# Kernel tuning notes

Hardware: AMD Instinct MI355X
Metric: run time of the kernel (lower is better)

Reference implementation:

```python
import math
import jax, jax.numpy as jnp
import numpy as np

B, T, C = 2, 2048, 2048
H, G = 16, 4          # n_head, n_group
HKV = H // G          # kv heads
HD = C // H           # head dim = 128

def setup_inputs() -> dict:
    key = jax.random.key(0)
    ks = jax.random.split(key, 4)
    s = 0.02  # realistic init scale
    return {
        "x": jax.random.normal(ks[0], (B, T, C), jnp.float32),
        "Wkv": jax.random.normal(ks[1], (C, 2 * C // G), jnp.float32) * s,
        "bkv": jnp.zeros((2 * C // G,), jnp.float32),
        "Wq": jax.random.normal(ks[2], (C, C), jnp.float32) * s,
        "bq": jnp.zeros((C,), jnp.float32),
        "Wp": jax.random.normal(ks[3], (C, C), jnp.float32) * s,
        "bp": jnp.zeros((C,), jnp.float32),
    }

def _expand_kv(t):
    # (B,T,HKV*HD) -> replicate each kv head G times -> (B,H,T,HD)
    t = t.reshape(B, T, HKV, HD)
    t = jnp.broadcast_to(t[:, :, None], (B, T, G, HKV, HD)).reshape(B, T, H, HD)
    return t.transpose(0, 2, 1, 3)

def reference(x, Wkv, bkv, Wq, bq, Wp, bp):
    kv = x @ Wkv + bkv                      # (B,T,2C/G)
    k, v = jnp.split(kv, 2, axis=-1)
    q = (x @ Wq + bq).reshape(B, T, H, HD).transpose(0, 2, 1, 3)  # (B,H,T,HD)
    k = _expand_kv(k)
    v = _expand_kv(v)
    att = jnp.einsum('bhqd,bhkd->bhqk', q, k) * (1.0 / math.sqrt(HD))
    mask = jnp.tril(jnp.ones((T, T), bool))
    att = jnp.where(mask, att, -jnp.inf)
    att = jax.nn.softmax(att, axis=-1)
    y = jnp.einsum('bhqk,bhkd->bhqd', att, v)
    y = y.transpose(0, 2, 1, 3).reshape(B, T, C)
    return y @ Wp + bp
```

## Files before the change

### kernel.cpp

```cpp
#include <hip/hip_runtime.h>

#define Bv 2
#define Tv 2048
#define Cv 2048
#define Hv 16
#define HKVv 4
#define HDv 128

typedef __attribute__((ext_vector_type(8))) __bf16 bf16x8;
typedef __attribute__((ext_vector_type(4))) float floatx4;

__device__ __forceinline__ unsigned short f2b(float f) {
  unsigned int x = __float_as_uint(f);
  x += 0x7fffu + ((x >> 16) & 1u);
  return (unsigned short)(x >> 16);
}

#define MFMA(a, b, c) __builtin_amdgcn_mfma_f32_16x16x32_bf16((a), (b), (c), 0, 0, 0)

__device__ __forceinline__ void gld_lds16(const void* g, void* l) {
  __builtin_amdgcn_global_load_lds((const __attribute__((address_space(1))) void*)g,
                                   (__attribute__((address_space(3))) void*)l, 16, 0, 0);
}

__global__ void cvt_kernel(const float* __restrict__ src, unsigned short* __restrict__ dst, int n4) {
  int i = blockIdx.x * blockDim.x + threadIdx.x;
  if (i < n4) {
    float4 f = ((const float4*)src)[i];
    ushort4 u;
    u.x = f2b(f.x); u.y = f2b(f.y); u.z = f2b(f.z); u.w = f2b(f.w);
    ((ushort4*)dst)[i] = u;
  }
}

__global__ void tcvt_kernel(const float* __restrict__ src, unsigned short* __restrict__ dst, int K, int N) {
  __shared__ float tile[32][33];
  int k0 = blockIdx.x * 32, n0 = blockIdx.y * 32;
  int tx = threadIdx.x, ty = threadIdx.y;
  for (int i = ty; i < 32; i += 8)
    tile[i][tx] = src[(size_t)(k0 + i) * N + n0 + tx];
  __syncthreads();
  for (int i = ty; i < 32; i += 8)
    dst[(size_t)(n0 + i) * K + k0 + tx] = f2b(tile[tx][i]);
}

__global__ __launch_bounds__(256) void gemm_qkv(
    const unsigned short* __restrict__ xb,
    const unsigned short* __restrict__ wq_t,
    const unsigned short* __restrict__ wkv_t,
    const float* __restrict__ bq, const float* __restrict__ bkv,
    unsigned short* __restrict__ qs,
    unsigned short* __restrict__ ks,
    unsigned short* __restrict__ vs) {
  __shared__ __align__(16) unsigned short Ash[2][128 * 32];
  __shared__ __align__(16) unsigned short Bsh[2][128 * 32];
  int tid = threadIdx.x;
  int wave = tid >> 6, lane = tid & 63;
  int c = lane & 15, quad = lane >> 4;
  int wr = (wave >> 1) * 64, wc = (wave & 1) * 64;
  int m0 = blockIdx.x * 128, n0 = blockIdx.y * 128;
  bool isq = (n0 < 2048);
  const unsigned short* wt = isq ? (wq_t + (size_t)n0 * 2048)
                                 : (wkv_t + (size_t)(n0 - 2048) * 2048);
  floatx4 zero4 = {0.f, 0.f, 0.f, 0.f};
  floatx4 acc[4][4];
#pragma unroll
  for (int i = 0; i < 4; i++)
#pragma unroll
    for (int j = 0; j < 4; j++) acc[i][j] = zero4;

  const unsigned short* Abase = xb + (size_t)m0 * 2048;
  int s0 = wave * 128 + lane, s1 = wave * 128 + 64 + lane;
  int r0 = s0 >> 2, kc0 = (s0 & 3) ^ (r0 & 3);
  int r1 = s1 >> 2, kc1 = (s1 & 3) ^ (r1 & 3);
  int swz3 = quad ^ (c & 3);
  int dA0 = (wave * 128) * 8, dA1 = (wave * 128 + 64) * 8;

  gld_lds16(Abase + (size_t)r0 * 2048 + kc0 * 8, &Ash[0][0] + dA0);
  gld_lds16(Abase + (size_t)r1 * 2048 + kc1 * 8, &Ash[0][0] + dA1);
  gld_lds16(wt + (size_t)r0 * 2048 + kc0 * 8, &Bsh[0][0] + dA0);
  gld_lds16(wt + (size_t)r1 * 2048 + kc1 * 8, &Bsh[0][0] + dA1);
  __syncthreads();

  for (int it = 0; it < 64; it++) {
    int cur = it & 1;
    if (it + 1 < 64) {
      int k1 = (it + 1) * 32;
      gld_lds16(Abase + (size_t)r0 * 2048 + k1 + kc0 * 8, &Ash[cur ^ 1][0] + dA0);
      gld_lds16(Abase + (size_t)r1 * 2048 + k1 + kc1 * 8, &Ash[cur ^ 1][0] + dA1);
      gld_lds16(wt + (size_t)r0 * 2048 + k1 + kc0 * 8, &Bsh[cur ^ 1][0] + dA0);
      gld_lds16(wt + (size_t)r1 * 2048 + k1 + kc1 * 8, &Bsh[cur ^ 1][0] + dA1);
    }
    bf16x8 af[4], bfv[4];
#pragma unroll
    for (int i = 0; i < 4; i++)
      af[i] = *(const bf16x8*)(&Ash[cur][(wr + i * 16 + c) * 32 + swz3 * 8]);
#pragma unroll
    for (int j = 0; j < 4; j++)
      bfv[j] = *(const bf16x8*)(&Bsh[cur][(wc + j * 16 + c) * 32 + swz3 * 8]);
#pragma unroll
    for (int i = 0; i < 4; i++)
#pragma unroll
      for (int j = 0; j < 4; j++)
        acc[i][j] = MFMA(af[i], bfv[j], acc[i][j]);
    __syncthreads();
  }

#pragma unroll
  for (int i = 0; i < 4; i++) {
#pragma unroll
    for (int j = 0; j < 4; j++) {
#pragma unroll
      for (int r = 0; r < 4; r++) {
        int m = m0 + wr + i * 16 + quad * 4 + r;
        int n = n0 + wc + j * 16 + c;
        int bidx = m >> 11, t = m & 2047;
        float val = acc[i][j][r];
        if (isq) {
          val = (val + bq[n]) * 0.08838834764831845f;
          int hh = n >> 7, d = n & 127;
          qs[((size_t)((bidx * Hv + hh) * Tv) + t) * HDv + d] = f2b(val);
        } else {
          int n2 = n - 2048;
          val += bkv[n2];
          if (n2 < 512) {
            int hh = n2 >> 7, d = n2 & 127;
            ks[((size_t)((bidx * HKVv + hh) * Tv) + t) * HDv + d] = f2b(val);
          } else {
            int n3 = n2 - 512;
            int hh = n3 >> 7, d = n3 & 127;
            vs[((size_t)((bidx * HKVv + hh) * HDv) + d) * Tv + t] = f2b(val);
          }
        }
      }
    }
  }
}

__global__ __launch_bounds__(256, 4) void attn_kernel(
    const unsigned short* __restrict__ qs,
    const unsigned short* __restrict__ ks,
    const unsigned short* __restrict__ vs,
    unsigned short* __restrict__ ys) {
  __shared__ __align__(16) unsigned short Ksh[2][32 * 128];
  __shared__ __align__(16) unsigned short Vsh[2][128 * 32];
  __shared__ __align__(16) unsigned short Psh[4][16 * 32];

  int x = blockIdx.x, h = blockIdx.y, b = blockIdx.z;
  int qt = (h & 8) ? (31 - x) : x;
  int hkv = h & (HKVv - 1);
  int tid = threadIdx.x;
  int wave = tid >> 6, lane = tid & 63;
  int c = lane & 15, quad = lane >> 4;
  int q0w = qt * 64 + wave * 16;
  int qrow = q0w + c;
  int swzK = c & 7, swzV = c & 3;

  const unsigned short* qptr = qs + ((size_t)((b * Hv + h) * Tv) + q0w) * HDv;
  const unsigned short* kbase = ks + (size_t)((b * HKVv + hkv) * Tv) * HDv;
  const unsigned short* vbase = vs + (size_t)((b * HKVv + hkv) * HDv) * Tv;

  bf16x8 qf[4];
#pragma unroll
  for (int kc = 0; kc < 4; kc++)
    qf[kc] = *(const bf16x8*)(qptr + (size_t)c * HDv + kc * 32 + quad * 8);

  floatx4 zero4 = {0.f, 0.f, 0.f, 0.f};
  floatx4 o[8];
#pragma unroll
  for (int dt = 0; dt < 8; dt++) o[dt] = zero4;
  float M = -1e30f, L = 0.f;

  unsigned short* Pw = &Psh[wave][0];

  int kOff[2], vOff[2];
#pragma unroll
  for (int i = 0; i < 2; i++) {
    int s = wave * 128 + i * 64 + lane;
    int rk = s >> 4, gk = (s & 15) ^ (rk & 7);
    kOff[i] = rk * 128 + gk * 8;
    int rv = s >> 2, gv = (s & 3) ^ (rv & 3);
    vOff[i] = rv * Tv + gv * 8;
  }
  int ldsBase = (wave * 128) * 8;

  int ntiles = 2 * qt + 2;

#pragma unroll
  for (int i = 0; i < 2; i++) gld_lds16(kbase + kOff[i], &Ksh[0][0] + ldsBase + i * 512);
#pragma unroll
  for (int i = 0; i < 2; i++) gld_lds16(vbase + vOff[i], &Vsh[0][0] + ldsBase + i * 512);
  __syncthreads();

  for (int kt = 0; kt < ntiles; kt++) {
    int kv0 = kt * 32;
    int cur = kt & 1;
    if (kt + 1 < ntiles) {
      int kv1 = (kt + 1) * 32;
#pragma unroll
      for (int i = 0; i < 2; i++)
        gld_lds16(kbase + (size_t)kv1 * 128 + kOff[i], &Ksh[cur ^ 1][0] + ldsBase + i * 512);
#pragma unroll
      for (int i = 0; i < 2; i++)
        gld_lds16(vbase + kv1 + vOff[i], &Vsh[cur ^ 1][0] + ldsBase + i * 512);
    }

    if (kv0 <= q0w + 15) {
      const unsigned short* Kb = &Ksh[cur][0];
      const unsigned short* Vb = &Vsh[cur][0];
      floatx4 st[2] = {zero4, zero4};
#pragma unroll
      for (int kc = 0; kc < 4; kc++) {
#pragma unroll
        for (int sub = 0; sub < 2; sub++) {
          bf16x8 kf = *(const bf16x8*)(&Kb[(sub * 16 + c) * 128 + (((kc * 4 + quad) ^ swzK) * 8)]);
          st[sub] = MFMA(kf, qf[kc], st[sub]);
        }
      }
      if (kv0 + 31 > q0w) {
#pragma unroll
        for (int sub = 0; sub < 2; sub++) {
          int kvb = kv0 + sub * 16 + quad * 4;
#pragma unroll
          for (int r = 0; r < 4; r++)
            if (kvb + r > qrow) st[sub][r] = -1e30f;
        }
      }
      float mx = -1e30f;
#pragma unroll
      for (int sub = 0; sub < 2; sub++)
        mx = fmaxf(mx, fmaxf(fmaxf(st[sub][0], st[sub][1]), fmaxf(st[sub][2], st[sub][3])));
      mx = fmaxf(mx, __shfl_xor(mx, 16));
      mx = fmaxf(mx, __shfl_xor(mx, 32));
      float Mn = fmaxf(M, mx);
      float al = __expf(M - Mn);
      M = Mn;
      float l = 0.f;
#pragma unroll
      for (int sub = 0; sub < 2; sub++) {
        float p0 = __expf(st[sub][0] - Mn);
        float p1 = __expf(st[sub][1] - Mn);
        float p2 = __expf(st[sub][2] - Mn);
        float p3 = __expf(st[sub][3] - Mn);
        l += (p0 + p1) + (p2 + p3);
        unsigned int lo = (unsigned int)f2b(p0) | ((unsigned int)f2b(p1) << 16);
        unsigned int hi = (unsigned int)f2b(p2) | ((unsigned int)f2b(p3) << 16);
        int g = (sub * 2 + (quad >> 1)) ^ swzV;
        *(uint2*)(&Pw[c * 32 + g * 8 + (quad & 1) * 4]) = make_uint2(lo, hi);
      }
      l += __shfl_xor(l, 16);
      l += __shfl_xor(l, 32);
      L = L * al + l;
#pragma unroll
      for (int dt = 0; dt < 8; dt++) o[dt] *= al;
      bf16x8 pf = *(const bf16x8*)(&Pw[c * 32 + ((quad ^ swzV) * 8)]);
#pragma unroll
      for (int dt = 0; dt < 8; dt++) {
        bf16x8 vf = *(const bf16x8*)(&Vb[(dt * 16 + c) * 32 + ((quad ^ swzV) * 8)]);
        o[dt] = MFMA(vf, pf, o[dt]);
      }
    }
    __syncthreads();
  }

  float Li = 1.0f / L;
  size_t rowbase = ((size_t)(b * Tv + qrow)) * Cv + h * HDv;
#pragma unroll
  for (int dt = 0; dt < 8; dt++) {
    unsigned int lo = (unsigned int)f2b(o[dt][0] * Li) | ((unsigned int)f2b(o[dt][1] * Li) << 16);
    unsigned int hi2 = (unsigned int)f2b(o[dt][2] * Li) | ((unsigned int)f2b(o[dt][3] * Li) << 16);
    *(uint2*)(&ys[rowbase + dt * 16 + quad * 4]) = make_uint2(lo, hi2);
  }
}

__global__ __launch_bounds__(256) void gemm_proj(
    const unsigned short* __restrict__ ys,
    const unsigned short* __restrict__ wp_t,
    const float* __restrict__ bp,
    float* __restrict__ out) {
  __shared__ __align__(16) unsigned short Ash[2][128 * 32];
  __shared__ __align__(16) unsigned short Bsh[2][128 * 32];
  int tid = threadIdx.x;
  int wave = tid >> 6, lane = tid & 63;
  int c = lane & 15, quad = lane >> 4;
  int wr = (wave >> 1) * 64, wc = (wave & 1) * 64;
  int m0 = blockIdx.x * 128, n0 = blockIdx.y * 128;
  floatx4 zero4 = {0.f, 0.f, 0.f, 0.f};
  floatx4 acc[4][4];
#pragma unroll
  for (int i = 0; i < 4; i++)
#pragma unroll
    for (int j = 0; j < 4; j++) acc[i][j] = zero4;

  const unsigned short* Abase = ys + (size_t)m0 * 2048;
  const unsigned short* Bbase = wp_t + (size_t)n0 * 2048;
  int s0 = wave * 128 + lane, s1 = wave * 128 + 64 + lane;
  int r0 = s0 >> 2, kc0 = (s0 & 3) ^ (r0 & 3);
  int r1 = s1 >> 2, kc1 = (s1 & 3) ^ (r1 & 3);
  int swz3 = quad ^ (c & 3);
  int dA0 = (wave * 128) * 8, dA1 = (wave * 128 + 64) * 8;

  gld_lds16(Abase + (size_t)r0 * 2048 + kc0 * 8, &Ash[0][0] + dA0);
  gld_lds16(Abase + (size_t)r1 * 2048 + kc1 * 8, &Ash[0][0] + dA1);
  gld_lds16(Bbase + (size_t)r0 * 2048 + kc0 * 8, &Bsh[0][0] + dA0);
  gld_lds16(Bbase + (size_t)r1 * 2048 + kc1 * 8, &Bsh[0][0] + dA1);
  __syncthreads();

  for (int it = 0; it < 64; it++) {
    int cur = it & 1;
    if (it + 1 < 64) {
      int k1 = (it + 1) * 32;
      gld_lds16(Abase + (size_t)r0 * 2048 + k1 + kc0 * 8, &Ash[cur ^ 1][0] + dA0);
      gld_lds16(Abase + (size_t)r1 * 2048 + k1 + kc1 * 8, &Ash[cur ^ 1][0] + dA1);
      gld_lds16(Bbase + (size_t)r0 * 2048 + k1 + kc0 * 8, &Bsh[cur ^ 1][0] + dA0);
      gld_lds16(Bbase + (size_t)r1 * 2048 + k1 + kc1 * 8, &Bsh[cur ^ 1][0] + dA1);
    }
    bf16x8 af[4], bfv[4];
#pragma unroll
    for (int i = 0; i < 4; i++)
      af[i] = *(const bf16x8*)(&Ash[cur][(wr + i * 16 + c) * 32 + swz3 * 8]);
#pragma unroll
    for (int j = 0; j < 4; j++)
      bfv[j] = *(const bf16x8*)(&Bsh[cur][(wc + j * 16 + c) * 32 + swz3 * 8]);
#pragma unroll
    for (int i = 0; i < 4; i++)
#pragma unroll
      for (int j = 0; j < 4; j++)
        acc[i][j] = MFMA(af[i], bfv[j], acc[i][j]);
    __syncthreads();
  }

#pragma unroll
  for (int i = 0; i < 4; i++) {
#pragma unroll
    for (int j = 0; j < 4; j++) {
#pragma unroll
      for (int r = 0; r < 4; r++) {
        int m = m0 + wr + i * 16 + quad * 4 + r;
        int n = n0 + wc + j * 16 + c;
        out[(size_t)m * 2048 + n] = acc[i][j][r] + bp[n];
      }
    }
  }
}

extern "C" void kernel_launch(void* const* d_in, const int* in_sizes, int n_in,
                              void* d_out, int out_size, void* d_ws, size_t ws_size,
                              hipStream_t stream) {
  (void)in_sizes; (void)n_in; (void)out_size; (void)ws_size;
  const float* x   = (const float*)d_in[0];
  const float* Wkv = (const float*)d_in[1];
  const float* bkv = (const float*)d_in[2];
  const float* Wq  = (const float*)d_in[3];
  const float* bq  = (const float*)d_in[4];
  const float* Wp  = (const float*)d_in[5];
  const float* bp  = (const float*)d_in[6];
  float* out = (float*)d_out;

  char* ws = (char*)d_ws;
  unsigned short* xb    = (unsigned short*)(ws + 0);
  unsigned short* wq_t  = (unsigned short*)(ws + 16777216);
  unsigned short* wkv_t = (unsigned short*)(ws + 25165824);
  unsigned short* wp_t  = (unsigned short*)(ws + 29360128);
  unsigned short* qs    = (unsigned short*)(ws + 37748736);
  unsigned short* ks    = (unsigned short*)(ws + 54525952);
  unsigned short* vs    = (unsigned short*)(ws + 58720256);
  unsigned short* ysbuf = (unsigned short*)(ws + 62914560);

  cvt_kernel<<<8192, 256, 0, stream>>>(x, xb, 2097152);
  tcvt_kernel<<<dim3(64, 64), dim3(32, 8), 0, stream>>>(Wq, wq_t, 2048, 2048);
  tcvt_kernel<<<dim3(64, 32), dim3(32, 8), 0, stream>>>(Wkv, wkv_t, 2048, 1024);
  tcvt_kernel<<<dim3(64, 64), dim3(32, 8), 0, stream>>>(Wp, wp_t, 2048, 2048);
  gemm_qkv<<<dim3(32, 24), 256, 0, stream>>>(xb, wq_t, wkv_t, bq, bkv, qs, ks, vs);
  attn_kernel<<<dim3(32, 16, 2), 256, 0, stream>>>(qs, ks, vs, ysbuf);
  gemm_proj<<<dim3(32, 16), 256, 0, stream>>>(ysbuf, wp_t, bp, out);
}
```

Measured before the change: 349.6 us.

## Switch attention to 32x32x16 MFMA with register-shuffled P, merge weight converts

```diff
diff --git a/kernel.cpp b/kernel.cpp
--- a/kernel.cpp
+++ b/kernel.cpp
@@ -8,7 +8,9 @@
 #define HDv 128
 
 typedef __attribute__((ext_vector_type(8))) __bf16 bf16x8;
+typedef __attribute__((ext_vector_type(4))) __bf16 bf16x4;
 typedef __attribute__((ext_vector_type(4))) float floatx4;
+typedef __attribute__((ext_vector_type(16))) float floatx16;
 
 __device__ __forceinline__ unsigned short f2b(float f) {
   unsigned int x = __float_as_uint(f);
@@ -17,6 +19,7 @@
 }
 
 #define MFMA(a, b, c) __builtin_amdgcn_mfma_f32_16x16x32_bf16((a), (b), (c), 0, 0, 0)
+#define MFMA32(a, b, c) __builtin_amdgcn_mfma_f32_32x32x16_bf16((a), (b), (c), 0, 0, 0)
 
 __device__ __forceinline__ void gld_lds16(const void* g, void* l) {
   __builtin_amdgcn_global_load_lds((const __attribute__((address_space(1))) void*)g,
@@ -33,15 +36,23 @@
   }
 }
 
-__global__ void tcvt_kernel(const float* __restrict__ src, unsigned short* __restrict__ dst, int K, int N) {
+__global__ void tcvt3_kernel(const float* __restrict__ Wq, const float* __restrict__ Wkv,
+                             const float* __restrict__ Wp,
+                             unsigned short* __restrict__ wq_t, unsigned short* __restrict__ wkv_t,
+                             unsigned short* __restrict__ wp_t) {
   __shared__ float tile[32][33];
+  int which = blockIdx.z;
+  const float* src = (which == 0) ? Wq : (which == 1) ? Wkv : Wp;
+  unsigned short* dst = (which == 0) ? wq_t : (which == 1) ? wkv_t : wp_t;
+  int N = (which == 1) ? 1024 : 2048;
+  if (which == 1 && blockIdx.y >= 32) return;
   int k0 = blockIdx.x * 32, n0 = blockIdx.y * 32;
   int tx = threadIdx.x, ty = threadIdx.y;
   for (int i = ty; i < 32; i += 8)
     tile[i][tx] = src[(size_t)(k0 + i) * N + n0 + tx];
   __syncthreads();
   for (int i = ty; i < 32; i += 8)
-    dst[(size_t)(n0 + i) * K + k0 + tx] = f2b(tile[tx][i]);
+    dst[(size_t)(n0 + i) * 2048 + k0 + tx] = f2b(tile[tx][i]);
 }
 
 __global__ __launch_bounds__(256) void gemm_qkv(
@@ -137,59 +148,56 @@
   }
 }
 
-__global__ __launch_bounds__(256, 4) void attn_kernel(
+__global__ __launch_bounds__(128, 2) void attn_kernel(
     const unsigned short* __restrict__ qs,
     const unsigned short* __restrict__ ks,
     const unsigned short* __restrict__ vs,
     unsigned short* __restrict__ ys) {
   __shared__ __align__(16) unsigned short Ksh[2][32 * 128];
   __shared__ __align__(16) unsigned short Vsh[2][128 * 32];
-  __shared__ __align__(16) unsigned short Psh[4][16 * 32];
 
   int x = blockIdx.x, h = blockIdx.y, b = blockIdx.z;
   int qt = (h & 8) ? (31 - x) : x;
   int hkv = h & (HKVv - 1);
   int tid = threadIdx.x;
   int wave = tid >> 6, lane = tid & 63;
-  int c = lane & 15, quad = lane >> 4;
-  int q0w = qt * 64 + wave * 16;
-  int qrow = q0w + c;
-  int swzK = c & 7, swzV = c & 3;
+  int q5 = lane & 31, hi = lane >> 5;
+  int q0w = qt * 64 + wave * 32;
+  int qrow = q0w + q5;
 
   const unsigned short* qptr = qs + ((size_t)((b * Hv + h) * Tv) + q0w) * HDv;
   const unsigned short* kbase = ks + (size_t)((b * HKVv + hkv) * Tv) * HDv;
   const unsigned short* vbase = vs + (size_t)((b * HKVv + hkv) * HDv) * Tv;
 
-  bf16x8 qf[4];
-#pragma unroll
-  for (int kc = 0; kc < 4; kc++)
-    qf[kc] = *(const bf16x8*)(qptr + (size_t)c * HDv + kc * 32 + quad * 8);
-
-  floatx4 zero4 = {0.f, 0.f, 0.f, 0.f};
-  floatx4 o[8];
-#pragma unroll
-  for (int dt = 0; dt < 8; dt++) o[dt] = zero4;
+  bf16x8 qf[8];
+#pragma unroll
+  for (int kc = 0; kc < 8; kc++)
+    qf[kc] = *(const bf16x8*)(qptr + (size_t)q5 * HDv + kc * 16 + hi * 8);
+
+  floatx16 o[4];
+#pragma unroll
+  for (int dt = 0; dt < 4; dt++)
+#pragma unroll
+    for (int r = 0; r < 16; r++) o[dt][r] = 0.f;
   float M = -1e30f, L = 0.f;
 
-  unsigned short* Pw = &Psh[wave][0];
-
-  int kOff[2], vOff[2];
-#pragma unroll
-  for (int i = 0; i < 2; i++) {
-    int s = wave * 128 + i * 64 + lane;
+  int kOff[4], vOff[4];
+#pragma unroll
+  for (int i = 0; i < 4; i++) {
+    int s = wave * 256 + i * 64 + lane;
     int rk = s >> 4, gk = (s & 15) ^ (rk & 7);
     kOff[i] = rk * 128 + gk * 8;
     int rv = s >> 2, gv = (s & 3) ^ (rv & 3);
     vOff[i] = rv * Tv + gv * 8;
   }
-  int ldsBase = (wave * 128) * 8;
+  int ldsBase = (wave * 256) * 8;
 
   int ntiles = 2 * qt + 2;
 
 #pragma unroll
-  for (int i = 0; i < 2; i++) gld_lds16(kbase + kOff[i], &Ksh[0][0] + ldsBase + i * 512);
-#pragma unroll
-  for (int i = 0; i < 2; i++) gld_lds16(vbase + vOff[i], &Vsh[0][0] + ldsBase + i * 512);
+  for (int i = 0; i < 4; i++) gld_lds16(kbase + kOff[i], &Ksh[0][0] + ldsBase + i * 512);
+#pragma unroll
+  for (int i = 0; i < 4; i++) gld_lds16(vbase + vOff[i], &Vsh[0][0] + ldsBase + i * 512);
   __syncthreads();
 
   for (int kt = 0; kt < ntiles; kt++) {
@@ -198,66 +206,78 @@
     if (kt + 1 < ntiles) {
       int kv1 = (kt + 1) * 32;
 #pragma unroll
-      for (int i = 0; i < 2; i++)
+      for (int i = 0; i < 4; i++)
         gld_lds16(kbase + (size_t)kv1 * 128 + kOff[i], &Ksh[cur ^ 1][0] + ldsBase + i * 512);
 #pragma unroll
-      for (int i = 0; i < 2; i++)
+      for (int i = 0; i < 4; i++)
         gld_lds16(vbase + kv1 + vOff[i], &Vsh[cur ^ 1][0] + ldsBase + i * 512);
     }
 
-    if (kv0 <= q0w + 15) {
+    if (kv0 <= q0w + 31) {
       const unsigned short* Kb = &Ksh[cur][0];
       const unsigned short* Vb = &Vsh[cur][0];
-      floatx4 st[2] = {zero4, zero4};
-#pragma unroll
-      for (int kc = 0; kc < 4; kc++) {
-#pragma unroll
-        for (int sub = 0; sub < 2; sub++) {
-          bf16x8 kf = *(const bf16x8*)(&Kb[(sub * 16 + c) * 128 + (((kc * 4 + quad) ^ swzK) * 8)]);
-          st[sub] = MFMA(kf, qf[kc], st[sub]);
+      floatx16 st;
+#pragma unroll
+      for (int r = 0; r < 16; r++) st[r] = 0.f;
+#pragma unroll
+      for (int kc = 0; kc < 8; kc++) {
+        bf16x8 kf = *(const bf16x8*)(&Kb[q5 * 128 + (((kc * 2 + hi) ^ (q5 & 7)) * 8)]);
+        st = MFMA32(kf, qf[kc], st);
+      }
+      if (kv0 + 31 > q0w) {
+        int kvb = kv0 + 4 * hi - qrow;
+#pragma unroll
+        for (int r = 0; r < 16; r++) {
+          int roff = (r & 3) + 8 * (r >> 2);
+          if (kvb + roff > 0) st[r] = -1e30f;
         }
       }
-      if (kv0 + 31 > q0w) {
-#pragma unroll
-        for (int sub = 0; sub < 2; sub++) {
-          int kvb = kv0 + sub * 16 + quad * 4;
-#pragma unroll
-          for (int r = 0; r < 4; r++)
-            if (kvb + r > qrow) st[sub][r] = -1e30f;
-        }
-      }
       float mx = -1e30f;
 #pragma unroll
-      for (int sub = 0; sub < 2; sub++)
-        mx = fmaxf(mx, fmaxf(fmaxf(st[sub][0], st[sub][1]), fmaxf(st[sub][2], st[sub][3])));
-      mx = fmaxf(mx, __shfl_xor(mx, 16));
+      for (int r = 0; r < 16; r++) mx = fmaxf(mx, st[r]);
       mx = fmaxf(mx, __shfl_xor(mx, 32));
       float Mn = fmaxf(M, mx);
       float al = __expf(M - Mn);
       M = Mn;
+      float p[16];
       float l = 0.f;
 #pragma unroll
-      for (int sub = 0; sub < 2; sub++) {
-        float p0 = __expf(st[sub][0] - Mn);
-        float p1 = __expf(st[sub][1] - Mn);
-        float p2 = __expf(st[sub][2] - Mn);
-        float p3 = __expf(st[sub][3] - Mn);
-        l += (p0 + p1) + (p2 + p3);
-        unsigned int lo = (unsigned int)f2b(p0) | ((unsigned int)f2b(p1) << 16);
-        unsigned int hi = (unsigned int)f2b(p2) | ((unsigned int)f2b(p3) << 16);
-        int g = (sub * 2 + (quad >> 1)) ^ swzV;
-        *(uint2*)(&Pw[c * 32 + g * 8 + (quad & 1) * 4]) = make_uint2(lo, hi);
-      }
-      l += __shfl_xor(l, 16);
+      for (int r = 0; r < 16; r++) {
+        p[r] = __expf(st[r] - Mn);
+        l += p[r];
+      }
       l += __shfl_xor(l, 32);
       L = L * al + l;
 #pragma unroll
-      for (int dt = 0; dt < 8; dt++) o[dt] *= al;
-      bf16x8 pf = *(const bf16x8*)(&Pw[c * 32 + ((quad ^ swzV) * 8)]);
-#pragma unroll
-      for (int dt = 0; dt < 8; dt++) {
-        bf16x8 vf = *(const bf16x8*)(&Vb[(dt * 16 + c) * 32 + ((quad ^ swzV) * 8)]);
-        o[dt] = MFMA(vf, pf, o[dt]);
+      for (int dt = 0; dt < 4; dt++)
+#pragma unroll
+        for (int r = 0; r < 16; r++) o[dt][r] *= al;
+      union Ub { bf16x4 v; uint2 u; };
+      uint2 pk[4];
+#pragma unroll
+      for (int m = 0; m < 4; m++) {
+        Ub t;
+        t.v = (bf16x4){(__bf16)p[m * 4 + 0], (__bf16)p[m * 4 + 1],
+                       (__bf16)p[m * 4 + 2], (__bf16)p[m * 4 + 3]};
+        pk[m] = t.u;
+      }
+#pragma unroll
+      for (int ksp = 0; ksp < 2; ksp++) {
+        int ml = 2 * ksp + hi;
+        int mr = 2 * ksp + (hi ^ 1);
+        unsigned int r0 = __shfl_xor((int)pk[mr].x, 32);
+        unsigned int r1 = __shfl_xor((int)pk[mr].y, 32);
+        unsigned int w0 = hi ? r0 : pk[ml].x;
+        unsigned int w1 = hi ? r1 : pk[ml].y;
+        unsigned int w2 = hi ? pk[ml].x : r0;
+        unsigned int w3 = hi ? pk[ml].y : r1;
+        union { unsigned int u[4]; bf16x8 v; } pf;
+        pf.u[0] = w0; pf.u[1] = w1; pf.u[2] = w2; pf.u[3] = w3;
+#pragma unroll
+        for (int dt = 0; dt < 4; dt++) {
+          bf16x8 vf = *(const bf16x8*)(&Vb[(dt * 32 + q5) * 32 + (((ksp * 2 + hi) ^ (q5 & 3)) * 8)]);
+          o[dt] = MFMA32(vf, pf.v, o[dt]);
+        }
       }
     }
     __syncthreads();
@@ -265,11 +285,17 @@
 
   float Li = 1.0f / L;
   size_t rowbase = ((size_t)(b * Tv + qrow)) * Cv + h * HDv;
-#pragma unroll
-  for (int dt = 0; dt < 8; dt++) {
-    unsigned int lo = (unsigned int)f2b(o[dt][0] * Li) | ((unsigned int)f2b(o[dt][1] * Li) << 16);
-    unsigned int hi2 = (unsigned int)f2b(o[dt][2] * Li) | ((unsigned int)f2b(o[dt][3] * Li) << 16);
-    *(uint2*)(&ys[rowbase + dt * 16 + quad * 4]) = make_uint2(lo, hi2);
+  union Ub2 { bf16x4 v; uint2 u; };
+#pragma unroll
+  for (int dt = 0; dt < 4; dt++) {
+#pragma unroll
+    for (int m = 0; m < 4; m++) {
+      int d = dt * 32 + 8 * m + 4 * hi;
+      Ub2 t;
+      t.v = (bf16x4){(__bf16)(o[dt][m * 4 + 0] * Li), (__bf16)(o[dt][m * 4 + 1] * Li),
+                     (__bf16)(o[dt][m * 4 + 2] * Li), (__bf16)(o[dt][m * 4 + 3] * Li)};
+      *(uint2*)(&ys[rowbase + d]) = t.u;
+    }
   }
 }
 
@@ -368,10 +394,8 @@
   unsigned short* ysbuf = (unsigned short*)(ws + 62914560);
 
   cvt_kernel<<<8192, 256, 0, stream>>>(x, xb, 2097152);
-  tcvt_kernel<<<dim3(64, 64), dim3(32, 8), 0, stream>>>(Wq, wq_t, 2048, 2048);
-  tcvt_kernel<<<dim3(64, 32), dim3(32, 8), 0, stream>>>(Wkv, wkv_t, 2048, 1024);
-  tcvt_kernel<<<dim3(64, 64), dim3(32, 8), 0, stream>>>(Wp, wp_t, 2048, 2048);
+  tcvt3_kernel<<<dim3(64, 64, 3), dim3(32, 8), 0, stream>>>(Wq, Wkv, Wp, wq_t, wkv_t, wp_t);
   gemm_qkv<<<dim3(32, 24), 256, 0, stream>>>(xb, wq_t, wkv_t, bq, bkv, qs, ks, vs);
-  attn_kernel<<<dim3(32, 16, 2), 256, 0, stream>>>(qs, ks, vs, ysbuf);
+  attn_kernel<<<dim3(32, 16, 2), 128, 0, stream>>>(qs, ks, vs, ysbuf);
   gemm_proj<<<dim3(32, 16), 256, 0, stream>>>(ysbuf, wp_t, bp, out);
 }
```

Result: slower. 364.4 us (+4.2%).
